# Kernel optimization log

Measured on AMD Instinct MI355X. Metric: run time of the kernel, lower is better.

Reference implementation:

```python
import jax, jax.numpy as jnp
import numpy as np

N_NODES = 100000
N_EDGES = 3200000
D_IN = 256
D_OUT = 256


def setup_inputs() -> dict:
    key = jax.random.key(0)
    k1, k2, k3, k4, k5, k6 = jax.random.split(key, 6)
    x = jax.random.normal(k1, (N_NODES, D_IN), dtype=jnp.float32)
    edge_row = jax.random.randint(k2, (N_EDGES,), 0, N_NODES, dtype=jnp.int32)
    edge_col = jax.random.randint(k3, (N_EDGES,), 0, N_NODES, dtype=jnp.int32)
    edge_val = jax.random.uniform(k4, (N_EDGES,), dtype=jnp.float32)
    # nn.Linear(in_features, out_features): weight [out, in], bias [out]
    bound = 1.0 / np.sqrt(D_IN)
    W = jax.random.uniform(k5, (D_OUT, D_IN), minval=-bound, maxval=bound, dtype=jnp.float32)
    b = jax.random.uniform(k6, (D_OUT,), minval=-bound, maxval=bound, dtype=jnp.float32)
    return {"x": x, "edge_row": edge_row, "edge_col": edge_col, "edge_val": edge_val, "W": W, "b": b}


def reference(x, edge_row, edge_col, edge_val, W, b):
    # torch.sparse.mm(adj, x): for each edge (r, c, v): agg[r] += v * x[c]
    gathered = edge_val[:, None] * x[edge_col]              # [E, D_IN]
    agg = jax.ops.segment_sum(gathered, edge_row, num_segments=N_NODES)  # [N, D_IN]
    # nn.Linear: agg @ W.T + b
    return jnp.einsum('nd,od->no', agg, W) + b
```

## Files before the change

### kernel.cpp

```cpp
#include <hip/hip_runtime.h>
#include <cstdint>
#include <cstddef>

#define D 256
#define NPB 32
#define SCAN_CHUNK 2048
#define BROWS 512
#define NBUCK 196
#define CHUNK_E 4096

typedef __attribute__((ext_vector_type(8))) short short8;
typedef __attribute__((ext_vector_type(4))) float floatx4;

__device__ __forceinline__ unsigned short f2bf(float f) {
    union { float f; unsigned int u; } cv; cv.f = f;
    unsigned int u = cv.u;
    unsigned int r = (u + 0x7fffu + ((u >> 16) & 1u)) >> 16;
    return (unsigned short)r;
}

__device__ __forceinline__ float bf2f(unsigned short s) {
    union { unsigned int u; float f; } cv;
    cv.u = ((unsigned int)s) << 16;
    return cv.f;
}

__global__ void k_prep(const int* __restrict__ erow, int* __restrict__ counts,
                       int* __restrict__ blkbins,
                       const float* __restrict__ x, unsigned short* __restrict__ xb,
                       const float* __restrict__ W, unsigned short* __restrict__ Wp,
                       int e, int n) {
    __shared__ int lb[NBUCK];
    const int tid = threadIdx.x;
    if (tid < NBUCK) lb[tid] = 0;
    __syncthreads();
    int gid = blockIdx.x * blockDim.x + tid;
    if (gid < e) {
        int r = erow[gid];
        atomicAdd(&counts[r], 1);
        atomicAdd(&lb[r >> 9], 1);
    }
    size_t i = (size_t)gid * 8;
    if (i < (size_t)n * D) {
        float4 a = *(const float4*)&x[i];
        float4 b = *(const float4*)&x[i + 4];
        short8 v;
        v[0] = (short)f2bf(a.x); v[1] = (short)f2bf(a.y);
        v[2] = (short)f2bf(a.z); v[3] = (short)f2bf(a.w);
        v[4] = (short)f2bf(b.x); v[5] = (short)f2bf(b.y);
        v[6] = (short)f2bf(b.z); v[7] = (short)f2bf(b.w);
        *(short8*)&xb[i] = v;
    }
    if (gid < 8192) {
        int ct = gid >> 9, rem = gid & 511;
        int ks = rem >> 6, ln = rem & 63;
        int q = ln >> 4, l = ln & 15;
        const float* src = &W[(size_t)(ct * 16 + l) * D + ks * 32 + q * 8];
        float4 c = *(const float4*)src;
        float4 d2 = *(const float4*)(src + 4);
        short8 w;
        w[0] = (short)f2bf(c.x); w[1] = (short)f2bf(c.y);
        w[2] = (short)f2bf(c.z); w[3] = (short)f2bf(c.w);
        w[4] = (short)f2bf(d2.x); w[5] = (short)f2bf(d2.y);
        w[6] = (short)f2bf(d2.z); w[7] = (short)f2bf(d2.w);
        *(short8*)&Wp[(size_t)gid * 8] = w;
    }
    __syncthreads();
    if (tid < NBUCK && lb[tid])
        atomicAdd(&blkbins[(blockIdx.x >> 4) * NBUCK + tid], lb[tid]);
}

__global__ void k_scan1(const int* __restrict__ counts, int* __restrict__ row_start,
                        int* __restrict__ blk_sums, int* __restrict__ dhist, int n) {
    __shared__ int sd[256];
    __shared__ int dh[256];
    int tid = threadIdx.x;
    dh[tid] = 0;
    int base = blockIdx.x * SCAN_CHUNK + tid * 8;
    int v[8];
    int s = 0;
#pragma unroll
    for (int i = 0; i < 8; ++i) {
        int idx = base + i;
        v[i] = (idx < n) ? counts[idx] : 0;
        s += v[i];
    }
    sd[tid] = s;
    __syncthreads();
    for (int off = 1; off < 256; off <<= 1) {
        int t = (tid >= off) ? sd[tid - off] : 0;
        __syncthreads();
        sd[tid] += t;
        __syncthreads();
    }
    int run = sd[tid] - s;
    if (tid == 255) blk_sums[blockIdx.x] = sd[255];
#pragma unroll
    for (int i = 0; i < 8; ++i) {
        int idx = base + i;
        if (idx < n) {
            row_start[idx] = run;
            atomicAdd(&dh[255 - min(v[i], 255)], 1);
        }
        run += v[i];
    }
    __syncthreads();
    if (dh[tid]) atomicAdd(&dhist[tid], dh[tid]);
}

__global__ void k_scan2(int* __restrict__ blk_sums, int* __restrict__ row_start,
                        const int* __restrict__ dhist, int* __restrict__ dcur,
                        int nch, int n) {
    __shared__ int sd[64];
    __shared__ int dh[256];
    int tid = threadIdx.x;
    if (tid < nch) sd[tid] = blk_sums[tid];
    dh[tid] = dhist[tid];
    __syncthreads();
    if (tid == 0) {
        int run = 0;
        for (int b = 0; b < nch; ++b) { int t = sd[b]; sd[b] = run; run += t; }
        row_start[n] = run;
    }
    __syncthreads();
    if (tid < nch) blk_sums[tid] = sd[tid];
    int own = dh[tid];
    for (int off = 1; off < 256; off <<= 1) {
        int t = (tid >= off) ? dh[tid - off] : 0;
        __syncthreads();
        dh[tid] += t;
        __syncthreads();
    }
    dcur[tid] = dh[tid] - own;
}

__global__ void k_scan3(int* __restrict__ row_start, const int* __restrict__ blk_sums, int n) {
    int i = blockIdx.x * blockDim.x + threadIdx.x;
    if (i < n) row_start[i] += blk_sums[i >> 11];
}

__global__ __launch_bounds__(256) void k_off(
    const int* __restrict__ blkbins, int* __restrict__ blkoff,
    const int* __restrict__ row_start, const int* __restrict__ counts,
    int* __restrict__ dcur, int* __restrict__ perm, int nchunk, int n) {
    __shared__ int sd[256];
    __shared__ int lh[256];
    __shared__ int lbase[256];
    const int tid = threadIdx.x;
    const int nch = (n + SCAN_CHUNK - 1) / SCAN_CHUNK;
    if (blockIdx.x < (unsigned)nch) {
        lh[tid] = 0;
        __syncthreads();
        const int base = blockIdx.x * SCAN_CHUNK + tid * 8;
        int b[8], rank[8];
#pragma unroll
        for (int i = 0; i < 8; ++i) {
            int idx = base + i;
            if (idx < n) {
                b[i] = 255 - min(counts[idx], 255);
                rank[i] = atomicAdd(&lh[b[i]], 1);
            }
        }
        __syncthreads();
        if (lh[tid]) lbase[tid] = atomicAdd(&dcur[tid], lh[tid]);
        __syncthreads();
#pragma unroll
        for (int i = 0; i < 8; ++i) {
            int idx = base + i;
            if (idx < n) perm[lbase[b[i]] + rank[i]] = idx;
        }
        __syncthreads();
    }
    const int bk = blockIdx.x;
    int carry = row_start[bk * BROWS];
    for (int c0 = 0; c0 < nchunk; c0 += 256) {
        int c = c0 + tid;
        int v = (c < nchunk) ? blkbins[c * NBUCK + bk] : 0;
        sd[tid] = v;
        __syncthreads();
        for (int off = 1; off < 256; off <<= 1) {
            int t = (tid >= off) ? sd[tid - off] : 0;
            __syncthreads();
            sd[tid] += t;
            __syncthreads();
        }
        if (c < nchunk) blkoff[c * NBUCK + bk] = carry + sd[tid] - v;
        int tot = sd[255];
        __syncthreads();
        carry += tot;
    }
}

__global__ __launch_bounds__(256) void k_stage(
    const int* __restrict__ erow, const int* __restrict__ ecol,
    const float* __restrict__ eval, const int* __restrict__ blkoff,
    int2* __restrict__ staged, int e) {
    __shared__ int lb[NBUCK];
    __shared__ int gb[NBUCK];
    __shared__ int sc[256];
    __shared__ unsigned char bid[CHUNK_E];
    __shared__ int2 ebuf[CHUNK_E];
    const int tid = threadIdx.x;
    if (tid < NBUCK) lb[tid] = 0;
    __syncthreads();
    const int ebase = blockIdx.x * CHUNK_E;
    int bk[16], rk[16];
#pragma unroll
    for (int i = 0; i < 16; ++i) {
        int idx = ebase + i * 256 + tid;
        bk[i] = -1;
        if (idx < e) {
            bk[i] = erow[idx] >> 9;
            rk[i] = atomicAdd(&lb[bk[i]], 1);
        }
    }
    __syncthreads();
    int v = (tid < NBUCK) ? lb[tid] : 0;
    sc[tid] = v;
    __syncthreads();
    for (int off = 1; off < 256; off <<= 1) {
        int t = (tid >= off) ? sc[tid - off] : 0;
        __syncthreads();
        sc[tid] += t;
        __syncthreads();
    }
    int loff = sc[tid] - v;
    if (tid < NBUCK) {
        lb[tid] = loff;
        gb[tid] = blkoff[blockIdx.x * NBUCK + tid] - loff;
    }
    __syncthreads();
#pragma unroll
    for (int i = 0; i < 16; ++i) {
        if (bk[i] >= 0) {
            int idx = ebase + i * 256 + tid;
            int slot = lb[bk[i]] + rk[i];
            int r = erow[idx];
            ebuf[slot] = make_int2(((r & (BROWS - 1)) << 17) | ecol[idx],
                                   __float_as_int(eval[idx]));
            bid[slot] = (unsigned char)bk[i];
        }
    }
    __syncthreads();
    const int cnt = min(e - ebase, CHUNK_E);
#pragma unroll
    for (int i = 0; i < 16; ++i) {
        int s = i * 256 + tid;
        if (s < cnt) staged[gb[bid[s]] + s] = ebuf[s];
    }
}

__global__ __launch_bounds__(256) void k_csr(
    const int2* __restrict__ staged, const int* __restrict__ row_start,
    int2* __restrict__ sedge, int n) {
    __shared__ int lcur[BROWS];
    const int b = blockIdx.x, tid = threadIdx.x;
    const int r0 = b * BROWS;
    const int rend = min(r0 + BROWS, n);
    for (int i = tid; i < rend - r0; i += 256) lcur[i] = row_start[r0 + i];
    __syncthreads();
    const int beg = row_start[r0];
    const int end = row_start[rend];
    for (int idx = beg + tid; idx < end; idx += 256) {
        int2 sv = staged[idx];
        int lr = ((unsigned)sv.x) >> 17;
        int p = atomicAdd(&lcur[lr], 1);
        sedge[p] = make_int2(sv.x & 0x1FFFF, sv.y);
    }
}

__global__ __launch_bounds__(256) void k_gg(
    const unsigned short* __restrict__ xb, const int2* __restrict__ sedge,
    const int* __restrict__ row_start, const int* __restrict__ perm,
    const unsigned short* __restrict__ Wp, const float* __restrict__ bias,
    float* __restrict__ out, int n) {
    __shared__ __align__(16) unsigned short aggl[32][264];
    __shared__ int pnl[32];
    const int tid = threadIdx.x;
    const int lane = tid & 63;
    const int wv = tid >> 6;
    const int base = blockIdx.x * NPB + wv * 8;

    int pn[8], ebeg[8], eend[8];
    int maxd = 0;
#pragma unroll
    for (int j = 0; j < 8; ++j) {
        pn[j] = perm[min(base + j, n - 1)];
        ebeg[j] = row_start[pn[j]];
        eend[j] = row_start[pn[j] + 1];
        maxd = max(maxd, eend[j] - ebeg[j]);
    }
    if (lane == 0) {
#pragma unroll
        for (int j = 0; j < 8; ++j) pnl[wv * 8 + j] = pn[j];
    }
    float4 acc[8];
#pragma unroll
    for (int j = 0; j < 8; ++j) acc[j] = make_float4(0.f, 0.f, 0.f, 0.f);

    for (int it = 0; it < maxd; ++it) {
        int2 ev[8];
        ushort4 xv[8];
#pragma unroll
        for (int j = 0; j < 8; ++j) {
            int e = ebeg[j] + it;
            int ec = max(min(e, eend[j] - 1), 0);
            ev[j] = sedge[ec];
        }
#pragma unroll
        for (int j = 0; j < 8; ++j) {
            xv[j] = *(const ushort4*)&xb[(size_t)ev[j].x * D + lane * 4];
        }
#pragma unroll
        for (int j = 0; j < 8; ++j) {
            float v = (ebeg[j] + it < eend[j]) ? __int_as_float(ev[j].y) : 0.f;
            acc[j].x += v * bf2f(xv[j].x);
            acc[j].y += v * bf2f(xv[j].y);
            acc[j].z += v * bf2f(xv[j].z);
            acc[j].w += v * bf2f(xv[j].w);
        }
    }
#pragma unroll
    for (int j = 0; j < 8; ++j) {
        ushort4 u;
        u.x = f2bf(acc[j].x);
        u.y = f2bf(acc[j].y);
        u.z = f2bf(acc[j].z);
        u.w = f2bf(acc[j].w);
        *(ushort4*)&aggl[wv * 8 + j][lane * 4] = u;
    }
    __syncthreads();

    const int q = lane >> 4, l = lane & 15;
    const int rt = wv >> 1;
    const int cb = (wv & 1) * 8;
    floatx4 gac[8];
#pragma unroll
    for (int i = 0; i < 8; ++i) gac[i] = (floatx4){0.f, 0.f, 0.f, 0.f};
#pragma unroll
    for (int ks = 0; ks < 8; ++ks) {
        short8 a = *(const short8*)&aggl[rt * 16 + l][ks * 32 + q * 8];
#pragma unroll
        for (int i = 0; i < 8; ++i) {
            short8 b = *(const short8*)&Wp[(size_t)(((cb + i) * 8 + ks) * 64 + lane) * 8];
            gac[i] = __builtin_amdgcn_mfma_f32_16x16x32_bf16(a, b, gac[i], 0, 0, 0);
        }
    }
#pragma unroll
    for (int i = 0; i < 8; ++i) {
        int o = (cb + i) * 16 + l;
        float bv = bias[o];
#pragma unroll
        for (int r = 0; r < 4; ++r) {
            int row = rt * 16 + q * 4 + r;
            if (base - wv * 8 + row < n)
                out[(size_t)pnl[row] * D + o] = gac[i][r] + bv;
        }
    }
}

extern "C" void kernel_launch(void* const* d_in, const int* in_sizes, int n_in,
                              void* d_out, int out_size, void* d_ws, size_t ws_size,
                              hipStream_t stream) {
    const float* x    = (const float*)d_in[0];
    const int*   erow = (const int*)d_in[1];
    const int*   ecol = (const int*)d_in[2];
    const float* eval = (const float*)d_in[3];
    const float* W    = (const float*)d_in[4];
    const float* bias = (const float*)d_in[5];
    float* out = (float*)d_out;

    const int n = in_sizes[0] / D;
    const int e = in_sizes[1];
    const int nchunk = (e + CHUNK_E - 1) / CHUNK_E;

    int* counts    = (int*)d_ws;
    int* dhist     = counts + n;
    int* blkbins   = dhist + 256;
    int* dcur      = blkbins + (size_t)nchunk * NBUCK;
    int* blk_sums  = dcur + 256;
    int* row_start = blk_sums + 64;
    int* perm      = row_start + n + 1;
    int* blkoff    = perm + n;
    int2* staged   = (int2*)(((uintptr_t)(blkoff + (size_t)nchunk * NBUCK) + 15) & ~(uintptr_t)15);
    int2* sedge    = staged + e;
    unsigned short* Wp = (unsigned short*)(sedge + e);
    unsigned short* xb = Wp + 65536;

    hipMemsetAsync(counts, 0, ((size_t)n + 256 + (size_t)nchunk * NBUCK) * sizeof(int), stream);

    const int nch = (n + SCAN_CHUNK - 1) / SCAN_CHUNK;

    k_prep<<<12500, 256, 0, stream>>>(erow, counts, blkbins, x, xb, W, Wp, e, n);
    k_scan1<<<nch, 256, 0, stream>>>(counts, row_start, blk_sums, dhist, n);
    k_scan2<<<1, 256, 0, stream>>>(blk_sums, row_start, dhist, dcur, nch, n);
    k_scan3<<<(n + 255) / 256, 256, 0, stream>>>(row_start, blk_sums, n);
    k_off<<<NBUCK, 256, 0, stream>>>(blkbins, blkoff, row_start, counts, dcur, perm, nchunk, n);
    k_stage<<<nchunk, 256, 0, stream>>>(erow, ecol, eval, blkoff, staged, e);
    k_csr<<<NBUCK, 256, 0, stream>>>(staged, row_start, sedge, n);
    k_gg<<<(n + NPB - 1) / NPB, 256, 0, stream>>>(xb, sedge, row_start, perm,
                                                  Wp, bias, out, n);
}
```

Baseline: 698.7 us.

## Derive per-row counts inside bucket CSR pass, dropping global per-row atomics and scans

Removes the 3.2M global atomicAdds on per-row counts in the prep kernel and the three-kernel global prefix scan. Row starts are now computed per 512-row bucket inside k_csr from a shared-memory histogram, with a small bucket-total scan (k_bscan) and a separate k_perm kernel for the degree-sorted permutation. This cuts global atomic traffic and kernel launches, but k_csr now reads each staged edge twice.

```diff
diff --git a/kernel.cpp b/kernel.cpp
--- a/kernel.cpp
+++ b/kernel.cpp
@@ -4,7 +4,6 @@
 
 #define D 256
 #define NPB 32
-#define SCAN_CHUNK 2048
 #define BROWS 512
 #define NBUCK 196
 #define CHUNK_E 4096
@@ -25,8 +24,7 @@
     return cv.f;
 }
 
-__global__ void k_prep(const int* __restrict__ erow, int* __restrict__ counts,
-                       int* __restrict__ blkbins,
+__global__ void k_prep(const int* __restrict__ erow, int* __restrict__ blkbins,
                        const float* __restrict__ x, unsigned short* __restrict__ xb,
                        const float* __restrict__ W, unsigned short* __restrict__ Wp,
                        int e, int n) {
@@ -35,11 +33,7 @@
     if (tid < NBUCK) lb[tid] = 0;
     __syncthreads();
     int gid = blockIdx.x * blockDim.x + tid;
-    if (gid < e) {
-        int r = erow[gid];
-        atomicAdd(&counts[r], 1);
-        atomicAdd(&lb[r >> 9], 1);
-    }
+    if (gid < e) atomicAdd(&lb[erow[gid] >> 9], 1);
     size_t i = (size_t)gid * 8;
     if (i < (size_t)n * D) {
         float4 a = *(const float4*)&x[i];
@@ -70,109 +64,13 @@
         atomicAdd(&blkbins[(blockIdx.x >> 4) * NBUCK + tid], lb[tid]);
 }
 
-__global__ void k_scan1(const int* __restrict__ counts, int* __restrict__ row_start,
-                        int* __restrict__ blk_sums, int* __restrict__ dhist, int n) {
-    __shared__ int sd[256];
-    __shared__ int dh[256];
-    int tid = threadIdx.x;
-    dh[tid] = 0;
-    int base = blockIdx.x * SCAN_CHUNK + tid * 8;
-    int v[8];
-    int s = 0;
-#pragma unroll
-    for (int i = 0; i < 8; ++i) {
-        int idx = base + i;
-        v[i] = (idx < n) ? counts[idx] : 0;
-        s += v[i];
-    }
-    sd[tid] = s;
-    __syncthreads();
-    for (int off = 1; off < 256; off <<= 1) {
-        int t = (tid >= off) ? sd[tid - off] : 0;
-        __syncthreads();
-        sd[tid] += t;
-        __syncthreads();
-    }
-    int run = sd[tid] - s;
-    if (tid == 255) blk_sums[blockIdx.x] = sd[255];
-#pragma unroll
-    for (int i = 0; i < 8; ++i) {
-        int idx = base + i;
-        if (idx < n) {
-            row_start[idx] = run;
-            atomicAdd(&dh[255 - min(v[i], 255)], 1);
-        }
-        run += v[i];
-    }
-    __syncthreads();
-    if (dh[tid]) atomicAdd(&dhist[tid], dh[tid]);
-}
-
-__global__ void k_scan2(int* __restrict__ blk_sums, int* __restrict__ row_start,
-                        const int* __restrict__ dhist, int* __restrict__ dcur,
-                        int nch, int n) {
-    __shared__ int sd[64];
-    __shared__ int dh[256];
-    int tid = threadIdx.x;
-    if (tid < nch) sd[tid] = blk_sums[tid];
-    dh[tid] = dhist[tid];
-    __syncthreads();
-    if (tid == 0) {
-        int run = 0;
-        for (int b = 0; b < nch; ++b) { int t = sd[b]; sd[b] = run; run += t; }
-        row_start[n] = run;
-    }
-    __syncthreads();
-    if (tid < nch) blk_sums[tid] = sd[tid];
-    int own = dh[tid];
-    for (int off = 1; off < 256; off <<= 1) {
-        int t = (tid >= off) ? dh[tid - off] : 0;
-        __syncthreads();
-        dh[tid] += t;
-        __syncthreads();
-    }
-    dcur[tid] = dh[tid] - own;
-}
-
-__global__ void k_scan3(int* __restrict__ row_start, const int* __restrict__ blk_sums, int n) {
-    int i = blockIdx.x * blockDim.x + threadIdx.x;
-    if (i < n) row_start[i] += blk_sums[i >> 11];
-}
-
 __global__ __launch_bounds__(256) void k_off(
     const int* __restrict__ blkbins, int* __restrict__ blkoff,
-    const int* __restrict__ row_start, const int* __restrict__ counts,
-    int* __restrict__ dcur, int* __restrict__ perm, int nchunk, int n) {
+    int* __restrict__ btot, int nchunk) {
     __shared__ int sd[256];
-    __shared__ int lh[256];
-    __shared__ int lbase[256];
-    const int tid = threadIdx.x;
-    const int nch = (n + SCAN_CHUNK - 1) / SCAN_CHUNK;
-    if (blockIdx.x < (unsigned)nch) {
-        lh[tid] = 0;
-        __syncthreads();
-        const int base = blockIdx.x * SCAN_CHUNK + tid * 8;
-        int b[8], rank[8];
-#pragma unroll
-        for (int i = 0; i < 8; ++i) {
-            int idx = base + i;
-            if (idx < n) {
-                b[i] = 255 - min(counts[idx], 255);
-                rank[i] = atomicAdd(&lh[b[i]], 1);
-            }
-        }
-        __syncthreads();
-        if (lh[tid]) lbase[tid] = atomicAdd(&dcur[tid], lh[tid]);
-        __syncthreads();
-#pragma unroll
-        for (int i = 0; i < 8; ++i) {
-            int idx = base + i;
-            if (idx < n) perm[lbase[b[i]] + rank[i]] = idx;
-        }
-        __syncthreads();
-    }
+    const int tid = threadIdx.x;
     const int bk = blockIdx.x;
-    int carry = row_start[bk * BROWS];
+    int carry = 0;
     for (int c0 = 0; c0 < nchunk; c0 += 256) {
         int c = c0 + tid;
         int v = (c < nchunk) ? blkbins[c * NBUCK + bk] : 0;
@@ -189,12 +87,33 @@
         __syncthreads();
         carry += tot;
     }
+    if (tid == 0) btot[bk] = carry;
+}
+
+__global__ void k_bscan(const int* __restrict__ btot, int* __restrict__ bstart,
+                        int* __restrict__ row_start, int n) {
+    __shared__ int sd[256];
+    const int tid = threadIdx.x;
+    int v = (tid < NBUCK) ? btot[tid] : 0;
+    sd[tid] = v;
+    __syncthreads();
+    for (int off = 1; off < 256; off <<= 1) {
+        int t = (tid >= off) ? sd[tid - off] : 0;
+        __syncthreads();
+        sd[tid] += t;
+        __syncthreads();
+    }
+    if (tid < NBUCK) bstart[tid] = sd[tid] - v;
+    if (tid == 255) {
+        bstart[NBUCK] = sd[255];
+        row_start[n] = sd[255];
+    }
 }
 
 __global__ __launch_bounds__(256) void k_stage(
     const int* __restrict__ erow, const int* __restrict__ ecol,
     const float* __restrict__ eval, const int* __restrict__ blkoff,
-    int2* __restrict__ staged, int e) {
+    const int* __restrict__ bstart, int2* __restrict__ staged, int e) {
     __shared__ int lb[NBUCK];
     __shared__ int gb[NBUCK];
     __shared__ int sc[256];
@@ -227,7 +146,7 @@
     int loff = sc[tid] - v;
     if (tid < NBUCK) {
         lb[tid] = loff;
-        gb[tid] = blkoff[blockIdx.x * NBUCK + tid] - loff;
+        gb[tid] = bstart[tid] + blkoff[blockIdx.x * NBUCK + tid] - loff;
     }
     __syncthreads();
 #pragma unroll
@@ -251,21 +170,104 @@
 }
 
 __global__ __launch_bounds__(256) void k_csr(
-    const int2* __restrict__ staged, const int* __restrict__ row_start,
-    int2* __restrict__ sedge, int n) {
-    __shared__ int lcur[BROWS];
+    const int2* __restrict__ staged, const int* __restrict__ bstart,
+    int* __restrict__ row_start, int* __restrict__ counts,
+    int* __restrict__ dhist, int2* __restrict__ sedge, int n) {
+    __shared__ int h[BROWS];
+    __shared__ int sc[256];
+    __shared__ int dh[256];
     const int b = blockIdx.x, tid = threadIdx.x;
     const int r0 = b * BROWS;
-    const int rend = min(r0 + BROWS, n);
-    for (int i = tid; i < rend - r0; i += 256) lcur[i] = row_start[r0 + i];
-    __syncthreads();
-    const int beg = row_start[r0];
-    const int end = row_start[rend];
+    h[tid] = 0; h[tid + 256] = 0; dh[tid] = 0;
+    __syncthreads();
+    const int beg = bstart[b];
+    const int end = bstart[b + 1];
+    for (int idx = beg + tid; idx < end; idx += 256) {
+        int lr = ((unsigned)staged[idx].x) >> 17;
+        atomicAdd(&h[lr], 1);
+    }
+    __syncthreads();
+    int a0 = h[tid], a1 = h[tid + 256];
+    sc[tid] = a0;
+    __syncthreads();
+    for (int off = 1; off < 256; off <<= 1) {
+        int t = (tid >= off) ? sc[tid - off] : 0;
+        __syncthreads();
+        sc[tid] += t;
+        __syncthreads();
+    }
+    int incl0 = sc[tid];
+    int tot0 = sc[255];
+    __syncthreads();
+    sc[tid] = a1;
+    __syncthreads();
+    for (int off = 1; off < 256; off <<= 1) {
+        int t = (tid >= off) ? sc[tid - off] : 0;
+        __syncthreads();
+        sc[tid] += t;
+        __syncthreads();
+    }
+    int incl1 = sc[tid];
+    __syncthreads();
+    int cur0 = beg + incl0 - a0;
+    int cur1 = beg + tot0 + incl1 - a1;
+    h[tid] = cur0;
+    h[tid + 256] = cur1;
+    if (r0 + tid < n) {
+        row_start[r0 + tid] = cur0;
+        counts[r0 + tid] = a0;
+        atomicAdd(&dh[255 - min(a0, 255)], 1);
+    }
+    if (r0 + 256 + tid < n) {
+        row_start[r0 + 256 + tid] = cur1;
+        counts[r0 + 256 + tid] = a1;
+        atomicAdd(&dh[255 - min(a1, 255)], 1);
+    }
+    __syncthreads();
+    if (dh[tid]) atomicAdd(&dhist[tid], dh[tid]);
     for (int idx = beg + tid; idx < end; idx += 256) {
         int2 sv = staged[idx];
         int lr = ((unsigned)sv.x) >> 17;
-        int p = atomicAdd(&lcur[lr], 1);
+        int p = atomicAdd(&h[lr], 1);
         sedge[p] = make_int2(sv.x & 0x1FFFF, sv.y);
+    }
+}
+
+__global__ __launch_bounds__(256) void k_perm(
+    const int* __restrict__ counts, const int* __restrict__ dhist,
+    int* __restrict__ dcur, int* __restrict__ perm, int n) {
+    __shared__ int st[256];
+    __shared__ int lh[256];
+    __shared__ int lbase[256];
+    const int tid = threadIdx.x;
+    lh[tid] = 0;
+    int dv = dhist[tid];
+    st[tid] = dv;
+    __syncthreads();
+    for (int off = 1; off < 256; off <<= 1) {
+        int t = (tid >= off) ? st[tid - off] : 0;
+        __syncthreads();
+        st[tid] += t;
+        __syncthreads();
+    }
+    int start = st[tid] - dv;
+    const int base = blockIdx.x * 2048 + tid * 8;
+    int bkt[8], rank[8];
+#pragma unroll
+    for (int i = 0; i < 8; ++i) {
+        int idx = base + i;
+        if (idx < n) {
+            bkt[i] = 255 - min(counts[idx], 255);
+            rank[i] = atomicAdd(&lh[bkt[i]], 1);
+        }
+    }
+    __syncthreads();
+    if (lh[tid]) lbase[tid] = start + atomicAdd(&dcur[tid], lh[tid]);
+    __syncthreads();
+#pragma unroll
+    for (int i = 0; i < 8; ++i) {
+        int idx = base + i;
+        if (idx < n) perm[lbase[bkt[i]] + rank[i]] = idx;
     }
 }
 
@@ -374,12 +376,13 @@
     const int e = in_sizes[1];
     const int nchunk = (e + CHUNK_E - 1) / CHUNK_E;
 
-    int* counts    = (int*)d_ws;
-    int* dhist     = counts + n;
-    int* blkbins   = dhist + 256;
-    int* dcur      = blkbins + (size_t)nchunk * NBUCK;
-    int* blk_sums  = dcur + 256;
-    int* row_start = blk_sums + 64;
+    int* blkbins   = (int*)d_ws;
+    int* dhist     = blkbins + (size_t)nchunk * NBUCK;
+    int* dcur      = dhist + 256;
+    int* btot      = dcur + 256;
+    int* bstart    = btot + NBUCK;
+    int* counts    = bstart + NBUCK + 1;
+    int* row_start = counts + n;
     int* perm      = row_start + n + 1;
     int* blkoff    = perm + n;
     int2* staged   = (int2*)(((uintptr_t)(blkoff + (size_t)nchunk * NBUCK) + 15) & ~(uintptr_t)15);
@@ -387,17 +390,14 @@
     unsigned short* Wp = (unsigned short*)(sedge + e);
     unsigned short* xb = Wp + 65536;
 
-    hipMemsetAsync(counts, 0, ((size_t)n + 256 + (size_t)nchunk * NBUCK) * sizeof(int), stream);
-
-    const int nch = (n + SCAN_CHUNK - 1) / SCAN_CHUNK;
-
-    k_prep<<<12500, 256, 0, stream>>>(erow, counts, blkbins, x, xb, W, Wp, e, n);
-    k_scan1<<<nch, 256, 0, stream>>>(counts, row_start, blk_sums, dhist, n);
-    k_scan2<<<1, 256, 0, stream>>>(blk_sums, row_start, dhist, dcur, nch, n);
-    k_scan3<<<(n + 255) / 256, 256, 0, stream>>>(row_start, blk_sums, n);
-    k_off<<<NBUCK, 256, 0, stream>>>(blkbins, blkoff, row_start, counts, dcur, perm, nchunk, n);
-    k_stage<<<nchunk, 256, 0, stream>>>(erow, ecol, eval, blkoff, staged, e);
-    k_csr<<<NBUCK, 256, 0, stream>>>(staged, row_start, sedge, n);
+    hipMemsetAsync(blkbins, 0, ((size_t)nchunk * NBUCK + 512) * sizeof(int), stream);
+
+    k_prep<<<12500, 256, 0, stream>>>(erow, blkbins, x, xb, W, Wp, e, n);
+    k_off<<<NBUCK, 256, 0, stream>>>(blkbins, blkoff, btot, nchunk);
+    k_bscan<<<1, 256, 0, stream>>>(btot, bstart, row_start, n);
+    k_stage<<<nchunk, 256, 0, stream>>>(erow, ecol, eval, blkoff, bstart, staged, e);
+    k_csr<<<NBUCK, 256, 0, stream>>>(staged, bstart, row_start, counts, dhist, sedge, n);
+    k_perm<<<49, 256, 0, stream>>>(counts, dhist, dcur, perm, n);
     k_gg<<<(n + NPB - 1) / NPB, 256, 0, stream>>>(xb, sedge, row_start, perm,
                                                   Wp, bias, out, n);
 }
```

After: 614.8 us. 12.0% less time.
